# Optimization experiments

Hardware: AMD Instinct MI355X
Metric: run time of the kernel (lower is better)

The kernel has to match this reference:

```python
import jax, jax.numpy as jnp
import numpy as np

R = 0.2                 # ball-query radius (Descriptor.r)
MAX_NBRS = 64           # CONFIG['Descriptor']['max_num_neighbors']


def setup_inputs() -> dict:
    key = jax.random.key(0)
    k1, k2, k3, k4, k5, k6 = jax.random.split(key, 6)
    N, F, M = 100000, 64, 2048
    x = jax.random.normal(k1, (N, F), dtype=jnp.float32)
    pos = jax.random.normal(k2, (N, 3), dtype=jnp.float32)
    batch = jnp.sort(jax.random.randint(k3, (N,), 0, 4, dtype=jnp.int64))
    key_idx = jax.random.randint(k4, (M,), 0, N, dtype=jnp.int64)
    # MLP params: Linear(F+3 -> 128), ReLU, Linear(128 -> 128)
    H = 128
    W1 = jax.random.normal(k5, (F + 3, H), dtype=jnp.float32) / np.sqrt(F + 3)
    b1 = jnp.zeros((H,), dtype=jnp.float32)
    W2 = jax.random.normal(k6, (H, H), dtype=jnp.float32) / np.sqrt(H)
    b2 = jnp.zeros((H,), dtype=jnp.float32)
    return {"x": x, "pos": pos, "W1": W1, "b1": b1, "W2": W2, "b2": b2,
            "batch": batch, "key_idx": key_idx}


def reference(x, pos, W1, b1, W2, b2, batch, key_idx):
    N = pos.shape[0]
    qpos = pos[key_idx]            # [M,3]
    qbatch = batch[key_idx]        # [M]

    # Brute-force ball query (what torch-cluster radius does under the hood):
    # squared distances via ||q||^2 + ||p||^2 - 2 q.p  -> [M,N]
    d2 = (jnp.sum(qpos * qpos, -1)[:, None]
          + jnp.sum(pos * pos, -1)[None, :]
          - 2.0 * qpos @ pos.T)
    valid = (d2 <= R * R) & (qbatch[:, None] == batch[None, :])   # [M,N]

    # Take the first MAX_NBRS valid neighbors per query (index order, as PyG).
    order_key = jnp.where(valid, jnp.arange(N)[None, :], N)       # invalid -> N
    neg_vals, idx = jax.lax.top_k(-order_key, MAX_NBRS)           # [M,K]
    valid_k = neg_vals > -N                                       # [M,K] real edge mask

    # PointNetConv message: nn(concat([x_j, pos_j - pos_i])), then max-aggregate.
    x_j = x[idx]                                  # [M,K,F] gather
    rel = pos[idx] - qpos[:, None, :]             # [M,K,3]
    h = jnp.concatenate([x_j, rel], axis=-1)      # [M,K,F+3]
    h = jax.nn.relu(h @ W1 + b1)
    h = h @ W2 + b2                               # [M,K,H]
    h = jnp.where(valid_k[..., None], h, -jnp.inf)
    out = jnp.max(h, axis=1)                      # [M,H] max-scatter
    out = jnp.where(jnp.any(valid_k, axis=1)[:, None], out, 0.0)

    # F.normalize(out, dim=-1)
    out = out / jnp.maximum(jnp.linalg.norm(out, axis=-1, keepdims=True), 1e-12)
    return out
```

## Files before the change

### kernel.cpp

```cpp
#include <hip/hip_runtime.h>
#include <math.h>

#define MAXK 64
#define HDIM 128
#define FDIM 64
#define NSPLIT 16

typedef __attribute__((ext_vector_type(8))) short bf16x8;
typedef __attribute__((ext_vector_type(4))) float f32x4;

__device__ __forceinline__ unsigned short f2bf(float f) {
    unsigned x = __float_as_uint(f);
    unsigned r = (x + 0x7fffu + ((x >> 16) & 1u)) >> 16;
    return (unsigned short)r;
}
__device__ __forceinline__ unsigned pk2(float a, float b) {
    return (unsigned)f2bf(a) | ((unsigned)f2bf(b) << 16);
}

__global__ __launch_bounds__(256) void prep_kernel(
    const float* __restrict__ W1, const float* __restrict__ W2,
    const float* __restrict__ pos, const int* __restrict__ batch, int N,
    unsigned short* __restrict__ W1bf, unsigned short* __restrict__ W2bf,
    float4* __restrict__ posq, int* __restrict__ bounds)
{
    int t = blockIdx.x * 256 + threadIdx.x;
    if (t < 1536) {
        int s = t;
        int cb = s / 192, rem = s % 192, ks = rem / 64, lane = rem % 64;
        int col = cb*16 + (lane & 15);
        int k0  = ks*32 + (lane >> 4)*8;
        unsigned short v[8];
        #pragma unroll
        for (int j = 0; j < 8; ++j) {
            int k = k0 + j;
            v[j] = (k < 67) ? f2bf(W1[k*HDIM + col]) : (unsigned short)0;
        }
        uint4 p;
        p.x = (unsigned)v[0] | ((unsigned)v[1] << 16);
        p.y = (unsigned)v[2] | ((unsigned)v[3] << 16);
        p.z = (unsigned)v[4] | ((unsigned)v[5] << 16);
        p.w = (unsigned)v[6] | ((unsigned)v[7] << 16);
        *reinterpret_cast<uint4*>(&W1bf[(size_t)s*8]) = p;
    } else if (t < 3584) {
        int s = t - 1536;
        int cb = s >> 8, ks = (s >> 6) & 3, lane = s & 63;
        int col = cb*16 + (lane & 15);
        int k0  = ks*32 + (lane >> 4)*8;
        unsigned short v[8];
        #pragma unroll
        for (int j = 0; j < 8; ++j) v[j] = f2bf(W2[(k0+j)*HDIM + col]);
        uint4 p;
        p.x = (unsigned)v[0] | ((unsigned)v[1] << 16);
        p.y = (unsigned)v[2] | ((unsigned)v[3] << 16);
        p.z = (unsigned)v[4] | ((unsigned)v[5] << 16);
        p.w = (unsigned)v[6] | ((unsigned)v[7] << 16);
        *reinterpret_cast<uint4*>(&W2bf[(size_t)s*8]) = p;
    } else if (t < 3584 + N) {
        int i = t - 3584;
        float px = pos[3*i+0], py = pos[3*i+1], pz = pos[3*i+2];
        float p2 = __fadd_rn(__fadd_rn(__fmul_rn(px,px), __fmul_rn(py,py)), __fmul_rn(pz,pz));
        posq[i] = make_float4(px, py, pz, p2);
    } else if (t < 3584 + N + 5) {
        int v = t - 3584 - N;
        int a = 0, e = N;
        while (a < e) { int mid = (a+e) >> 1; if (batch[mid] < v) a = mid+1; else e = mid; }
        bounds[v] = a;
    }
}

__global__ __launch_bounds__(64) void scan_kernel(
    const float4* __restrict__ posq, const int* __restrict__ batch,
    const int* __restrict__ key_idx, const int* __restrict__ bounds,
    int* __restrict__ lists, int* __restrict__ lcnt)
{
    int b = blockIdx.x;
    int m = b >> 4, w = b & 15;
    int lane = threadIdx.x;

    int qi = key_idx[m];
    int qb = batch[qi];
    float4 q4 = posq[qi];
    float qx = q4.x, qy = q4.y, qz = q4.z, q2 = q4.w;

    int lo = bounds[qb], hi = bounds[qb+1];

    const float R2 = 0.04f;

    int seg   = hi - lo;
    int qlen  = (seg + NSPLIT - 1) >> 4;
    int start = lo + w*qlen;
    int qend  = min(start + qlen, hi);

    int lc = 0;
    for (int base = start; base < qend && lc < MAXK; base += 256) {
        unsigned long long mk[4]; bool vv[4]; int jj[4];
        #pragma unroll
        for (int sub = 0; sub < 4; ++sub) {
            int j = base + sub*64 + lane;
            bool v = false;
            if (j < qend) {
                float4 p = posq[j];
                float dt = __fadd_rn(__fadd_rn(__fmul_rn(qx,p.x), __fmul_rn(qy,p.y)), __fmul_rn(qz,p.z));
                float d2 = __fsub_rn(__fadd_rn(q2, p.w), __fmul_rn(2.0f, dt));
                v = (d2 <= R2);
            }
            mk[sub] = __ballot(v); vv[sub] = v; jj[sub] = j;
        }
        #pragma unroll
        for (int sub = 0; sub < 4; ++sub) {
            if (vv[sub]) {
                int slot = lc + (int)__popcll(mk[sub] & ((1ull << lane) - 1ull));
                if (slot < MAXK) lists[b*MAXK + slot] = jj[sub];
            }
            lc += (int)__popcll(mk[sub]);
        }
    }
    if (lane == 0) lcnt[b] = min(lc, MAXK);
}

__global__ __launch_bounds__(256) void mlp_kernel(
    const float* __restrict__ x, const float4* __restrict__ posq,
    const unsigned short* __restrict__ W1bf, const unsigned short* __restrict__ W2bf,
    const float* __restrict__ b1, const float* __restrict__ b2,
    const int* __restrict__ key_idx,
    const int* __restrict__ lists, const int* __restrict__ lcnt,
    float* __restrict__ out, int M)
{
    __shared__ __align__(16) unsigned short h_lds[4*16*128];
    __shared__ float pmax_s[4][HDIM];
    __shared__ float rsum[2];

    int m   = blockIdx.x;
    int tid = threadIdx.x;
    int lane = tid & 63, w = tid >> 6;
    int colq = lane & 15, rq = lane >> 4;

    int qi = key_idx[m];
    float4 q4 = posq[qi];

    int row = w*16 + colq;
    int cnt = 0, src = -1;
    #pragma unroll
    for (int t = 0; t < NSPLIT; ++t) {
        int ct = lcnt[m*NSPLIT + t];
        if (row >= cnt && row - cnt < ct) src = (m*NSPLIT + t)*MAXK + (row - cnt);
        cnt += ct;
    }
    if (cnt > MAXK) cnt = MAXK;

    union { bf16x8 v; uint4 u; } A0, A1, A2;
    A0.u = make_uint4(0,0,0,0); A1.u = A0.u; A2.u = A0.u;
    if (row < cnt) {
        int idx = lists[src];
        const float4* xp = reinterpret_cast<const float4*>(x + (size_t)idx*FDIM + rq*8);
        float4 u0 = xp[0], u1 = xp[1];
        const float4* xq = reinterpret_cast<const float4*>(x + (size_t)idx*FDIM + 32 + rq*8);
        float4 u2 = xq[0], u3 = xq[1];
        A0.u.x = pk2(u0.x, u0.y); A0.u.y = pk2(u0.z, u0.w);
        A0.u.z = pk2(u1.x, u1.y); A0.u.w = pk2(u1.z, u1.w);
        A1.u.x = pk2(u2.x, u2.y); A1.u.y = pk2(u2.z, u2.w);
        A1.u.z = pk2(u3.x, u3.y); A1.u.w = pk2(u3.z, u3.w);
        if (rq == 0) {
            float4 p = posq[idx];
            A2.u.x = pk2(p.x - q4.x, p.y - q4.y);
            A2.u.y = pk2(p.z - q4.z, 0.f);
        }
    }

    const bf16x8* W1f = reinterpret_cast<const bf16x8*>(W1bf);
    const bf16x8* W2f = reinterpret_cast<const bf16x8*>(W2bf);

    #pragma unroll
    for (int cb = 0; cb < 8; ++cb) {
        f32x4 c = {0.f, 0.f, 0.f, 0.f};
        c = __builtin_amdgcn_mfma_f32_16x16x32_bf16(A0.v, W1f[(cb*3+0)*64 + lane], c, 0, 0, 0);
        c = __builtin_amdgcn_mfma_f32_16x16x32_bf16(A1.v, W1f[(cb*3+1)*64 + lane], c, 0, 0, 0);
        c = __builtin_amdgcn_mfma_f32_16x16x32_bf16(A2.v, W1f[(cb*3+2)*64 + lane], c, 0, 0, 0);
        int col = cb*16 + colq;
        float bias = b1[col];
        #pragma unroll
        for (int reg = 0; reg < 4; ++reg) {
            int r = rq*4 + reg;
            float h = fmaxf(c[reg] + bias, 0.f);
            h_lds[w*2048 + r*128 + (col ^ ((r & 7) << 3))] = f2bf(h);
        }
    }

    int r = colq, swz = (r & 7) << 3;
    bf16x8 g0 = *reinterpret_cast<const bf16x8*>(&h_lds[w*2048 + r*128 + ((  0 + rq*8) ^ swz)]);
    bf16x8 g1 = *reinterpret_cast<const bf16x8*>(&h_lds[w*2048 + r*128 + (( 32 + rq*8) ^ swz)]);
    bf16x8 g2 = *reinterpret_cast<const bf16x8*>(&h_lds[w*2048 + r*128 + (( 64 + rq*8) ^ swz)]);
    bf16x8 g3 = *reinterpret_cast<const bf16x8*>(&h_lds[w*2048 + r*128 + (( 96 + rq*8) ^ swz)]);
    #pragma unroll
    for (int cb = 0; cb < 8; ++cb) {
        f32x4 c = {0.f, 0.f, 0.f, 0.f};
        c = __builtin_amdgcn_mfma_f32_16x16x32_bf16(g0, W2f[(cb*4+0)*64 + lane], c, 0, 0, 0);
        c = __builtin_amdgcn_mfma_f32_16x16x32_bf16(g1, W2f[(cb*4+1)*64 + lane], c, 0, 0, 0);
        c = __builtin_amdgcn_mfma_f32_16x16x32_bf16(g2, W2f[(cb*4+2)*64 + lane], c, 0, 0, 0);
        c = __builtin_amdgcn_mfma_f32_16x16x32_bf16(g3, W2f[(cb*4+3)*64 + lane], c, 0, 0, 0);
        int col = cb*16 + colq;
        float bias = b2[col];
        float mx = -INFINITY;
        #pragma unroll
        for (int reg = 0; reg < 4; ++reg) {
            int rr = w*16 + rq*4 + reg;
            float val = c[reg] + bias;
            if (rr < cnt) mx = fmaxf(mx, val);
        }
        mx = fmaxf(mx, __shfl_xor(mx, 16, 64));
        mx = fmaxf(mx, __shfl_xor(mx, 32, 64));
        if (rq == 0) pmax_s[w][col] = mx;
    }
    __syncthreads();

    int c = tid & 127, g = tid >> 7;
    float v = fmaxf(fmaxf(pmax_s[0][c], pmax_s[1][c]),
                    fmaxf(pmax_s[2][c], pmax_s[3][c]));
    if (cnt == 0) v = 0.f;
    float s = (g == 0) ? v*v : 0.f;
    #pragma unroll
    for (int o = 32; o > 0; o >>= 1) s += __shfl_xor(s, o, 64);
    if (g == 0 && (tid & 63) == 0) rsum[tid >> 6] = s;
    __syncthreads();
    if (g == 0) {
        float nrm = fmaxf(sqrtf(rsum[0] + rsum[1]), 1e-12f);
        out[(size_t)m*HDIM + c] = v / nrm;
    }
}

extern "C" void kernel_launch(void* const* d_in, const int* in_sizes, int n_in,
                              void* d_out, int out_size, void* d_ws, size_t ws_size,
                              hipStream_t stream)
{
    const float* x       = (const float*)d_in[0];
    const float* pos     = (const float*)d_in[1];
    const float* W1      = (const float*)d_in[2];
    const float* b1      = (const float*)d_in[3];
    const float* W2      = (const float*)d_in[4];
    const float* b2      = (const float*)d_in[5];
    const int*   batch   = (const int*)d_in[6];
    const int*   key_idx = (const int*)d_in[7];

    int N = in_sizes[6];
    int M = in_sizes[7];

    unsigned short* W1bf = (unsigned short*)d_ws;
    unsigned short* W2bf = W1bf + 12288;
    float4* posq  = (float4*)(W2bf + 16384);
    int* bounds   = (int*)(posq + N);
    int* lists    = bounds + 8;
    int* lcnt     = lists + (size_t)M * NSPLIT * MAXK;

    int prep_blocks = (3584 + N + 5 + 255) / 256;
    prep_kernel<<<prep_blocks, 256, 0, stream>>>(W1, W2, pos, batch, N,
                                                 W1bf, W2bf, posq, bounds);
    scan_kernel<<<M*NSPLIT, 64, 0, stream>>>(posq, batch, key_idx, bounds,
                                             lists, lcnt);
    mlp_kernel<<<M, 256, 0, stream>>>(x, posq, W1bf, W2bf, b1, b2, key_idx,
                                      lists, lcnt, (float*)d_out, M);
}
```

Before: 143.4 us.

## Group queries by batch and scan LDS-tiled points per query thread

The prep kernel now builds per-batch query lists with atomics and computes batch boundaries from adjacent-element comparisons instead of binary search. The scan kernel changes from one wave per query-split, where each wave streams every candidate point from global memory, to blocks of 256 same-batch queries. Each block loads tiles of points into LDS once and every thread tests its own query against the tile, so point loads are shared across 256 queries. NSPLIT rises to 32. The cost is per-thread divergent writes to the neighbour lists, the loss of per-wave early exit at 64 found, and a memset for the counters.

```diff
diff --git a/kernel.cpp b/kernel.cpp
--- a/kernel.cpp
+++ b/kernel.cpp
@@ -4,7 +4,9 @@
 #define MAXK 64
 #define HDIM 128
 #define FDIM 64
-#define NSPLIT 16
+#define NSPLIT 32
+#define NB 4
+#define QBLK 256
 
 typedef __attribute__((ext_vector_type(8))) short bf16x8;
 typedef __attribute__((ext_vector_type(4))) float f32x4;
@@ -20,9 +22,11 @@
 
 __global__ __launch_bounds__(256) void prep_kernel(
     const float* __restrict__ W1, const float* __restrict__ W2,
-    const float* __restrict__ pos, const int* __restrict__ batch, int N,
+    const float* __restrict__ pos, const int* __restrict__ batch,
+    const int* __restrict__ key_idx, int N, int M,
     unsigned short* __restrict__ W1bf, unsigned short* __restrict__ W2bf,
-    float4* __restrict__ posq, int* __restrict__ bounds)
+    float4* __restrict__ posq, int* __restrict__ bounds,
+    int* __restrict__ qn, int* __restrict__ qlist)
 {
     int t = blockIdx.x * 256 + threadIdx.x;
     if (t < 1536) {
@@ -61,62 +65,83 @@
         float px = pos[3*i+0], py = pos[3*i+1], pz = pos[3*i+2];
         float p2 = __fadd_rn(__fadd_rn(__fmul_rn(px,px), __fmul_rn(py,py)), __fmul_rn(pz,pz));
         posq[i] = make_float4(px, py, pz, p2);
-    } else if (t < 3584 + N + 5) {
-        int v = t - 3584 - N;
-        int a = 0, e = N;
-        while (a < e) { int mid = (a+e) >> 1; if (batch[mid] < v) a = mid+1; else e = mid; }
-        bounds[v] = a;
-    }
-}
-
-__global__ __launch_bounds__(64) void scan_kernel(
-    const float4* __restrict__ posq, const int* __restrict__ batch,
-    const int* __restrict__ key_idx, const int* __restrict__ bounds,
+    } else if (t < 3584 + 2*N) {
+        int i = t - 3584 - N;
+        int b1 = batch[i];
+        if (i == 0) {
+            for (int v = 0; v <= b1; ++v) bounds[v] = 0;
+        } else {
+            int b0 = batch[i-1];
+            for (int v = b0+1; v <= b1; ++v) bounds[v] = i;
+        }
+        if (i == N-1) {
+            for (int v = b1+1; v <= NB; ++v) bounds[v] = N;
+        }
+    } else if (t < 3584 + 2*N + M) {
+        int m = t - 3584 - 2*N;
+        int qb = batch[key_idx[m]];
+        int slot = atomicAdd(&qn[qb], 1);
+        qlist[qb*M + slot] = m;
+    }
+}
+
+__global__ __launch_bounds__(256) void scan_kernel(
+    const float4* __restrict__ posq, const int* __restrict__ key_idx,
+    const int* __restrict__ bounds, const int* __restrict__ qn,
+    const int* __restrict__ qlist, int M,
     int* __restrict__ lists, int* __restrict__ lcnt)
 {
-    int b = blockIdx.x;
-    int m = b >> 4, w = b & 15;
-    int lane = threadIdx.x;
-
-    int qi = key_idx[m];
-    int qb = batch[qi];
-    float4 q4 = posq[qi];
-    float qx = q4.x, qy = q4.y, qz = q4.z, q2 = q4.w;
-
-    int lo = bounds[qb], hi = bounds[qb+1];
+    __shared__ __align__(16) float4 tile[QBLK];
+
+    int blk = blockIdx.x;
+    int s  = blk & (NSPLIT-1);
+    int g  = (blk >> 5) & 7;
+    int bb = blk >> 8;
+
+    int nq = qn[bb];
+    if (g*QBLK >= nq) return;
+
+    int tid = threadIdx.x;
+    int qslot = g*QBLK + tid;
+    int me = (qslot < nq) ? qlist[bb*M + qslot] : -1;
+
+    float qx = 0.f, qy = 0.f, qz = 0.f, q2 = 0.f;
+    if (me >= 0) {
+        float4 q4 = posq[key_idx[me]];
+        qx = q4.x; qy = q4.y; qz = q4.z; q2 = q4.w;
+    }
 
     const float R2 = 0.04f;
 
-    int seg   = hi - lo;
-    int qlen  = (seg + NSPLIT - 1) >> 4;
-    int start = lo + w*qlen;
+    int lo = bounds[bb], hi = bounds[bb+1];
+    int seg  = hi - lo;
+    int qlen = (seg + NSPLIT - 1) >> 5;
+    int start = lo + s*qlen;
     int qend  = min(start + qlen, hi);
 
     int lc = 0;
-    for (int base = start; base < qend && lc < MAXK; base += 256) {
-        unsigned long long mk[4]; bool vv[4]; int jj[4];
-        #pragma unroll
-        for (int sub = 0; sub < 4; ++sub) {
-            int j = base + sub*64 + lane;
-            bool v = false;
-            if (j < qend) {
-                float4 p = posq[j];
+    int outbase = (me >= 0) ? (me*NSPLIT + s)*MAXK : 0;
+
+    for (int t0 = start; t0 < qend; t0 += QBLK) {
+        int navail = min(QBLK, qend - t0);
+        if (t0 + tid < qend) tile[tid] = posq[t0 + tid];
+        __syncthreads();
+        bool active = (me >= 0) && (lc < MAXK);
+        if (__builtin_amdgcn_ballot_w64(active)) {
+            #pragma unroll 4
+            for (int tt = 0; tt < navail; ++tt) {
+                float4 p = tile[tt];
                 float dt = __fadd_rn(__fadd_rn(__fmul_rn(qx,p.x), __fmul_rn(qy,p.y)), __fmul_rn(qz,p.z));
                 float d2 = __fsub_rn(__fadd_rn(q2, p.w), __fmul_rn(2.0f, dt));
-                v = (d2 <= R2);
+                if (active && d2 <= R2 && lc < MAXK) {
+                    lists[outbase + lc] = t0 + tt;
+                    ++lc;
+                }
             }
-            mk[sub] = __ballot(v); vv[sub] = v; jj[sub] = j;
-        }
-        #pragma unroll
-        for (int sub = 0; sub < 4; ++sub) {
-            if (vv[sub]) {
-                int slot = lc + (int)__popcll(mk[sub] & ((1ull << lane) - 1ull));
-                if (slot < MAXK) lists[b*MAXK + slot] = jj[sub];
-            }
-            lc += (int)__popcll(mk[sub]);
-        }
-    }
-    if (lane == 0) lcnt[b] = min(lc, MAXK);
+        }
+        __syncthreads();
+    }
+    if (me >= 0) lcnt[me*NSPLIT + s] = lc;
 }
 
 __global__ __launch_bounds__(256) void mlp_kernel(
@@ -249,14 +274,21 @@
     unsigned short* W2bf = W1bf + 12288;
     float4* posq  = (float4*)(W2bf + 16384);
     int* bounds   = (int*)(posq + N);
-    int* lists    = bounds + 8;
+    int* qn       = bounds + 8;
+    int* qlist    = qn + 8;
+    int* lists    = qlist + (size_t)NB * M;
     int* lcnt     = lists + (size_t)M * NSPLIT * MAXK;
 
-    int prep_blocks = (3584 + N + 5 + 255) / 256;
-    prep_kernel<<<prep_blocks, 256, 0, stream>>>(W1, W2, pos, batch, N,
-                                                 W1bf, W2bf, posq, bounds);
-    scan_kernel<<<M*NSPLIT, 64, 0, stream>>>(posq, batch, key_idx, bounds,
-                                             lists, lcnt);
+    hipMemsetAsync(qn, 0, 8 * sizeof(int), stream);
+
+    int prep_threads = 3584 + 2*N + M;
+    prep_kernel<<<(prep_threads + 255)/256, 256, 0, stream>>>(
+        W1, W2, pos, batch, key_idx, N, M, W1bf, W2bf, posq, bounds, qn, qlist);
+
+    int scan_blocks = NB * ((M + QBLK - 1)/QBLK) * NSPLIT;
+    scan_kernel<<<scan_blocks, 256, 0, stream>>>(posq, key_idx, bounds, qn,
+                                                 qlist, M, lists, lcnt);
+
     mlp_kernel<<<M, 256, 0, stream>>>(x, posq, W1bf, W2bf, b1, b2, key_idx,
                                       lists, lcnt, (float*)d_out, M);
 }
```

New measurement: 195.5 us. 36.4% more time.
